# Kernel tuning notes

Measured on AMD Instinct MI355X. Metric: run time of the kernel, lower is better.

The kernel has to match this reference:

```python
import jax, jax.numpy as jnp
import numpy as np


def _binarize(x):
    # sign-binarization with straight-through estimator (matches torch .data trick)
    return x + jax.lax.stop_gradient(jnp.sign(x) - x)


def _conv(x, w):
    # x: NCHW, w: OIHW, stride 1, no padding (padding handled explicitly)
    return jax.lax.conv_general_dilated(
        x, w, window_strides=(1, 1), padding='VALID',
        dimension_numbers=('NCHW', 'OIHW', 'NCHW'))


def _hardtanh(x):
    return jnp.clip(x, -1.0, 1.0)


def _maxpool2(x):
    # 2x2 max pool, stride 2, over spatial dims of NCHW
    return jax.lax.reduce_window(
        x, -jnp.inf, jax.lax.max,
        window_dimensions=(1, 1, 2, 2), window_strides=(1, 1, 2, 2),
        padding='VALID')


def setup_inputs() -> dict:
    key = jax.random.key(0)
    kx, k1, k2, k3, k4 = jax.random.split(key, 5)
    x = jax.random.normal(kx, (32, 3, 512, 512), dtype=jnp.float32)
    w1 = jax.random.normal(k1, (8, 3, 3, 3), dtype=jnp.float32) * 0.1
    w2 = jax.random.normal(k2, (16, 8, 3, 3), dtype=jnp.float32) * 0.1
    w3 = jax.random.normal(k3, (32, 16, 3, 3), dtype=jnp.float32) * 0.1
    w4 = jax.random.normal(k4, (2, 32, 3, 3), dtype=jnp.float32) * 0.1
    return {'x': x, 'w1': w1, 'w2': w2, 'w3': w3, 'w4': w4}


def reference(x, w1, w2, w3, w4):
    # p0: ConstantPad2d(1, value=1)
    h = jnp.pad(x, ((0, 0), (0, 0), (1, 1), (1, 1)), constant_values=1.0)
    # features1: BinarizeConv2d(3,8) -- input has 3 channels so NOT binarized;
    # weights are sign-binarized. Then Hardtanh, MaxPool2d(2,2).
    h = _maxpool2(_hardtanh(_conv(h, _binarize(w1))))          # [B,8,256,256]
    # features2..4: binarize activations (C != 3) and weights, conv, hardtanh
    h = _hardtanh(_conv(_binarize(h), _binarize(w2)))          # [B,16,254,254]
    h = _hardtanh(_conv(_binarize(h), _binarize(w3)))          # [B,32,252,252]
    h = _hardtanh(_conv(_binarize(h), _binarize(w4)))          # [B,2,250,250]
    return h.reshape(h.shape[0], -1)                           # [B, 125000]
```

## Files before the change

kernel.cpp:

```cpp
#include <hip/hip_runtime.h>
#include <hip/hip_bf16.h>
#include <cstdint>


typedef __attribute__((ext_vector_type(2)))  float f32x2;
typedef __attribute__((ext_vector_type(4)))  int int4v;
typedef __attribute__((ext_vector_type(16))) int int16v;

#define WOFF_W2M 0
#define WOFF_W3M 10240
#define WOFF_W4M 20480
#define WOFF_W1D 30720
#define WEIGHTS_BYTES 32768

#define A1_PB (2*256*256*4)
#define A2_PB (4*254*254*4)

__device__ __forceinline__ int fsign(float w) {
    return (w > 0.f) ? 1 : ((w < 0.f) ? -1 : 0);
}

__device__ __forceinline__ void pkfma_lo(f32x2& acc, f32x2 w, f32x2 v) {
    asm("v_pk_fma_f32 %0, %1, %2, %0 op_sel:[0,0,0] op_sel_hi:[1,0,1]"
        : "+v"(acc) : "s"(w), "v"(v));
}
__device__ __forceinline__ void pkfma_hi(f32x2& acc, f32x2 w, f32x2 v) {
    asm("v_pk_fma_f32 %0, %1, %2, %0 op_sel:[0,1,0] op_sel_hi:[1,1,1]"
        : "+v"(acc) : "s"(w), "v"(v));
}

__global__ __launch_bounds__(256) void kprep(const float* __restrict__ w1,
                                             const float* __restrict__ w2,
                                             const float* __restrict__ w3,
                                             const float* __restrict__ w4,
                                             int* __restrict__ w2m,
                                             int* __restrict__ w3m,
                                             int* __restrict__ w4m,
                                             f32x2* __restrict__ w1d) {
    int tid = threadIdx.x;
    int b = blockIdx.x;
    if (b == 0) {
        for (int idx = tid; idx < 576; idx += 256) {
            int t = idx / 64, l = idx % 64;
            int oc = l & 31, icb = (l >> 5) * 16;
            int wd[4] = {0, 0, 0, 0};
            for (int j = 0; j < 16; ++j) {
                int ic = icb + j;
                int s = (oc < 16 && ic < 8) ? fsign(w2[(oc * 8 + ic) * 9 + t]) : 0;
                wd[j >> 2] |= (s & 0xff) << (8 * (j & 3));
            }
            w2m[idx * 4 + 0] = wd[0]; w2m[idx * 4 + 1] = wd[1];
            w2m[idx * 4 + 2] = wd[2]; w2m[idx * 4 + 3] = wd[3];
        }
    } else if (b == 1) {
        for (int idx = tid; idx < 576; idx += 256) {
            int t = idx / 64, l = idx % 64;
            int oc = l & 31, icb = (l >> 5) * 16;
            int wd[4] = {0, 0, 0, 0};
            for (int j = 0; j < 16; ++j) {
                int ic = icb + j;
                int s = (ic < 16) ? fsign(w3[(oc * 16 + ic) * 9 + t]) : 0;
                wd[j >> 2] |= (s & 0xff) << (8 * (j & 3));
            }
            w3m[idx * 4 + 0] = wd[0]; w3m[idx * 4 + 1] = wd[1];
            w3m[idx * 4 + 2] = wd[2]; w3m[idx * 4 + 3] = wd[3];
        }
    } else {
        for (int idx = tid; idx < 576; idx += 256) {
            int t = idx / 64, l = idx % 64;
            int oc = l & 31, icb = (l >> 5) * 16;
            int wd[4] = {0, 0, 0, 0};
            for (int j = 0; j < 16; ++j) {
                int ic = icb + j;
                int s = (oc < 2) ? fsign(w4[(oc * 32 + ic) * 9 + t]) : 0;
                wd[j >> 2] |= (s & 0xff) << (8 * (j & 3));
            }
            w4m[idx * 4 + 0] = wd[0]; w4m[idx * 4 + 1] = wd[1];
            w4m[idx * 4 + 2] = wd[2]; w4m[idx * 4 + 3] = wd[3];
        }
        for (int i = tid; i < 128; i += 256) {
            int op = i / 32, t = i % 32;
            f32x2 pr = {0.f, 0.f};
            if (t < 27) {
                float wa = w1[(2 * op) * 27 + t];
                float wbv = w1[(2 * op + 1) * 27 + t];
                pr[0] = (wa > 0.f) ? 1.f : ((wa < 0.f) ? -1.f : 0.f);
                pr[1] = (wbv > 0.f) ? 1.f : ((wbv < 0.f) ? -1.f : 0.f);
            }
            w1d[i] = pr;
        }
    }
}

__global__ __launch_bounds__(128, 4) void k1(const float* __restrict__ x,
                                             const f32x2* __restrict__ w1d,
                                             uint32_t* __restrict__ a1, int n0) {
    int tx = threadIdx.x;
    int oy = blockIdx.y;
    int ln = blockIdx.z;
    const float* xn = x + (size_t)(n0 + ln) * 3 * 512 * 512;

    int iy0 = 2 * oy - 1;
    int xb  = 4 * tx;

    f32x2 P[3][4][3];

    if (oy > 0 && oy < 255 && tx > 0 && tx < 127) {
#pragma unroll
        for (int ic = 0; ic < 3; ++ic) {
            const float* xc = xn + (size_t)ic * 512 * 512;
#pragma unroll
            for (int r = 0; r < 4; ++r) {
                const float* rp = xc + (size_t)(iy0 + r) * 512 + xb;
                float  lft = rp[-1];
                float4 m   = *(const float4*)rp;
                float  rgt = rp[4];
                P[ic][r][0] = (f32x2){lft, m.x};
                P[ic][r][1] = (f32x2){m.y, m.z};
                P[ic][r][2] = (f32x2){m.w, rgt};
            }
        }
    } else {
        for (int ic = 0; ic < 3; ++ic) {
            const float* xc = xn + (size_t)ic * 512 * 512;
#pragma unroll
            for (int r = 0; r < 4; ++r) {
                int iy = iy0 + r;
                bool yok = ((unsigned)iy < 512u);
                float t[6];
#pragma unroll
                for (int c = 0; c < 6; ++c) {
                    int ix = xb - 1 + c;
                    t[c] = (yok && ((unsigned)ix < 512u))
                               ? xc[(size_t)iy * 512 + ix] : 1.0f;
                }
                P[ic][r][0] = (f32x2){t[0], t[1]};
                P[ic][r][1] = (f32x2){t[2], t[3]};
                P[ic][r][2] = (f32x2){t[4], t[5]};
            }
        }
    }

#define PKTAP(ACC, ROW, COL)                                         \
    do {                                                             \
        if (((COL) & 1) == 0) pkfma_lo(ACC, ww, P[ic][ROW][(COL) >> 1]); \
        else                  pkfma_hi(ACC, ww, P[ic][ROW][(COL) >> 1]); \
    } while (0)

    uint64_t dallA = 0, dallB = 0;
#pragma unroll 1
    for (int op = 0; op < 4; ++op) {
        const f32x2* wb = w1d + op * 32;
        f32x2 wop[27];
#pragma unroll
        for (int t = 0; t < 27; ++t) wop[t] = wb[t];

        f32x2 aA00 = {0.f, 0.f}, aA01 = {0.f, 0.f};
        f32x2 aA10 = {0.f, 0.f}, aA11 = {0.f, 0.f};
        f32x2 aB00 = {0.f, 0.f}, aB01 = {0.f, 0.f};
        f32x2 aB10 = {0.f, 0.f}, aB11 = {0.f, 0.f};
#pragma unroll
        for (int ky = 0; ky < 3; ++ky) {
#pragma unroll
            for (int kx = 0; kx < 3; ++kx) {
#pragma unroll
                for (int ic = 0; ic < 3; ++ic) {
                    f32x2 ww = wop[ic * 9 + ky * 3 + kx];
                    PKTAP(aA00, ky + 0, kx + 0);
                    PKTAP(aA01, ky + 0, kx + 1);
                    PKTAP(aA10, ky + 1, kx + 0);
                    PKTAP(aA11, ky + 1, kx + 1);
                    PKTAP(aB00, ky + 0, kx + 2);
                    PKTAP(aB01, ky + 0, kx + 3);
                    PKTAP(aB10, ky + 1, kx + 2);
                    PKTAP(aB11, ky + 1, kx + 3);
                }
            }
        }
        float mA0 = fmaxf(fmaxf(aA00[0], aA01[0]), fmaxf(aA10[0], aA11[0]));
        float mA1 = fmaxf(fmaxf(aA00[1], aA01[1]), fmaxf(aA10[1], aA11[1]));
        float mB0 = fmaxf(fmaxf(aB00[0], aB01[0]), fmaxf(aB10[0], aB11[0]));
        float mB1 = fmaxf(fmaxf(aB00[1], aB01[1]), fmaxf(aB10[1], aB11[1]));
        int sA0 = (mA0 > 0.f) ? 1 : ((mA0 < 0.f) ? -1 : 0);
        int sA1 = (mA1 > 0.f) ? 1 : ((mA1 < 0.f) ? -1 : 0);
        int sB0 = (mB0 > 0.f) ? 1 : ((mB0 < 0.f) ? -1 : 0);
        int sB1 = (mB1 > 0.f) ? 1 : ((mB1 < 0.f) ? -1 : 0);
        dallA |= (uint64_t)(uint32_t)(sA0 & 0xff) << (8 * (2 * op));
        dallA |= (uint64_t)(uint32_t)(sA1 & 0xff) << (8 * (2 * op + 1));
        dallB |= (uint64_t)(uint32_t)(sB0 & 0xff) << (8 * (2 * op));
        dallB |= (uint64_t)(uint32_t)(sB1 & 0xff) << (8 * (2 * op + 1));
    }
#undef PKTAP

    size_t base = (((size_t)ln * 2) * 256 + oy) * 256 + 2 * tx;
    uint2 v0, v1;
    v0.x = (uint32_t)dallA;         v0.y = (uint32_t)dallB;
    v1.x = (uint32_t)(dallA >> 32); v1.y = (uint32_t)(dallB >> 32);
    *(uint2*)(a1 + base)             = v0;
    *(uint2*)(a1 + base + 256 * 256) = v1;
}

__global__ __launch_bounds__(256) void kconv2(const uint32_t* __restrict__ ain,
                                              const int* __restrict__ wm,
                                              uint32_t* __restrict__ aout) {
    __shared__ uint32_t stb[10][36][2];
    int w    = threadIdx.x >> 6;
    int lane = threadIdx.x & 63;
    int x0 = blockIdx.x * 32;
    int y0 = blockIdx.y * 8;
    int ln = blockIdx.z;

    const int4v* wmv = (const int4v*)wm;
    int4v bfr[9];
#pragma unroll
    for (int t = 0; t < 9; ++t) bfr[t] = wmv[t * 64 + lane];

    const uint32_t* abase = ain + (size_t)ln * 2 * 256 * 256;
    for (int idx = threadIdx.x; idx < 10 * 36 * 2; idx += 256) {
        int icg = idx & 1;
        int r2 = idx >> 1;
        int xx = r2 % 36, row = r2 / 36;
        int gy = y0 + row, gx = x0 + xx;
        uint32_t val = 0;
        if (xx < 34 && gx < 256 && gy < 256)
            val = abase[((size_t)icg * 256 + gy) * 256 + gx];
        stb[row][xx][icg] = val;
    }
    __syncthreads();

    int xl = lane & 31;
    int h  = lane >> 5;

#pragma unroll
    for (int ry = 0; ry < 2; ++ry) {
        int yy = y0 + 2 * w + ry;
        int16v acc = {};
#pragma unroll
        for (int ky = 0; ky < 3; ++ky) {
#pragma unroll
            for (int kx = 0; kx < 3; ++kx) {
                uint32_t d0 = stb[2 * w + ry + ky][xl + kx][0];
                uint32_t d1 = stb[2 * w + ry + ky][xl + kx][1];
                int4v a; a[0] = (int)d0; a[1] = (int)d1; a[2] = 0; a[3] = 0;
                acc = __builtin_amdgcn_mfma_i32_32x32x32_i8(bfr[ky * 3 + kx], a, acc, 0, 0, 0);
            }
        }
        bool ok = (yy < 254) && (x0 + xl < 254);
#pragma unroll
        for (int g = 0; g < 4; ++g) {
            int ocg = 2 * g + h;
            if (ocg < 4 && ok) {
                uint32_t dw = 0;
#pragma unroll
                for (int j = 0; j < 4; ++j) {
                    int v = min(max(acc[4 * g + j], -1), 1);
                    dw |= (uint32_t)(v & 0xff) << (8 * j);
                }
                aout[(((size_t)ln * 4 + ocg) * 254 + yy) * 254 + x0 + xl] = dw;
            }
        }
    }
}

__global__ __launch_bounds__(256) void kconv34(const uint32_t* __restrict__ a2,
                                               const int* __restrict__ w3m,
                                               const int* __restrict__ w4m,
                                               float* __restrict__ out, int n0) {
    __shared__ uint32_t sA2[12][68][4];
    __shared__ uint32_t sA3[10 * 66 * 9];
    int w    = threadIdx.x >> 6;
    int lane = threadIdx.x & 63;
    int xl = lane & 31;
    int h  = lane >> 5;
    int x0 = blockIdx.x * 62;
    int y0 = blockIdx.y * 8;
    int ln = blockIdx.z;

    const int4v* wmv3 = (const int4v*)w3m;
    int4v bfr[9];
#pragma unroll
    for (int t = 0; t < 9; ++t) bfr[t] = wmv3[t * 64 + lane];

    const uint32_t* abase = a2 + (size_t)ln * 4 * 254 * 254;
    for (int idx = threadIdx.x; idx < 12 * 64 * 4; idx += 256) {
        int row = idx >> 8;
        int xx  = (idx >> 2) & 63;
        int icg = idx & 3;
        int gy = y0 + row, gx = x0 + xx;
        uint32_t val = 0;
        if (gy < 254 && gx < 254)
            val = abase[((size_t)icg * 254 + gy) * 254 + gx];
        sA2[row][xx][icg] = val;
    }
    if (threadIdx.x < 96) {
        int row = threadIdx.x >> 3;
        int xx  = 64 + ((threadIdx.x >> 2) & 1);
        int icg = threadIdx.x & 3;
        int gy = y0 + row, gx = x0 + xx;
        uint32_t val = 0;
        if (gy < 254 && gx < 254)
            val = abase[((size_t)icg * 254 + gy) * 254 + gx];
        sA2[row][xx][icg] = val;
    }
    __syncthreads();

#pragma unroll
    for (int t5 = 0; t5 < 5; ++t5) {
        int t = t5 * 4 + w;
        int row = t >> 1, ct = t & 1;
        int16v acc = {};
#pragma unroll
        for (int ky = 0; ky < 3; ++ky) {
#pragma unroll
            for (int kx = 0; kx < 3; ++kx) {
                int4v a = *(const int4v*)&sA2[row + ky][ct * 32 + xl + kx][0];
                acc = __builtin_amdgcn_mfma_i32_32x32x32_i8(bfr[ky * 3 + kx], a, acc, 0, 0, 0);
            }
        }
        int pbase = (row * 66 + ct * 32 + xl) * 9;
#pragma unroll
        for (int g = 0; g < 4; ++g) {
            uint32_t dw = 0;
#pragma unroll
            for (int j = 0; j < 4; ++j) {
                int v = min(max(acc[4 * g + j], -1), 1);
                dw |= (uint32_t)(v & 0xff) << (8 * j);
            }
            sA3[pbase + 2 * g + h] = dw;
        }
    }

    const int4v* wmv4 = (const int4v*)w4m;
    int4v bf4[9];
#pragma unroll
    for (int t = 0; t < 9; ++t) bf4[t] = wmv4[t * 64 + lane];
    __syncthreads();

    size_t gn = (size_t)(n0 + ln);
#pragma unroll
    for (int t4 = 0; t4 < 4; ++t4) {
        int t = t4 * 4 + w;
        int y = t >> 1, ct2 = t & 1;
        int gy = y0 + y;
        int16v acc = {};
#pragma unroll
        for (int ky = 0; ky < 3; ++ky) {
#pragma unroll
            for (int kx = 0; kx < 3; ++kx) {
                const uint32_t* pb = &sA3[((y + ky) * 66 + ct2 * 32 + xl + kx) * 9 + h * 4];
                int4v bv;
                bv[0] = (int)pb[0]; bv[1] = (int)pb[1];
                bv[2] = (int)pb[2]; bv[3] = (int)pb[3];
                acc = __builtin_amdgcn_mfma_i32_32x32x32_i8(bf4[ky * 3 + kx], bv, acc, 0, 0, 0);
            }
        }
        if (h == 0) {
            int lx = ct2 * 32 + xl;
            if (lx < 62 && x0 + lx < 250 && gy < 250) {
                float v0 = fminf(fmaxf((float)acc[0], -1.f), 1.f);
                float v1 = fminf(fmaxf((float)acc[1], -1.f), 1.f);
                out[((gn * 2 + 0) * 250 + gy) * 250 + x0 + lx] = v0;
                out[((gn * 2 + 1) * 250 + gy) * 250 + x0 + lx] = v1;
            }
        }
    }
}

extern "C" void kernel_launch(void* const* d_in, const int* in_sizes, int n_in,
                              void* d_out, int out_size, void* d_ws, size_t ws_size,
                              hipStream_t stream) {
    const float* x  = (const float*)d_in[0];
    const float* w1 = (const float*)d_in[1];
    const float* w2 = (const float*)d_in[2];
    const float* w3 = (const float*)d_in[3];
    const float* w4 = (const float*)d_in[4];
    char* ws = (char*)d_ws;

    int*   w2m = (int*)(ws + WOFF_W2M);
    int*   w3m = (int*)(ws + WOFF_W3M);
    int*   w4m = (int*)(ws + WOFF_W4M);
    f32x2* w1d = (f32x2*)(ws + WOFF_W1D);
    float* out = (float*)d_out;

    size_t per = (size_t)A1_PB + (size_t)A2_PB;
    int NC = 32;
    while (NC > 1 && (size_t)WEIGHTS_BYTES + (size_t)NC * per > ws_size) NC >>= 1;

    uint32_t* A1 = (uint32_t*)(ws + WEIGHTS_BYTES);
    uint32_t* A2 = (uint32_t*)(ws + WEIGHTS_BYTES + (size_t)NC * A1_PB);

    kprep<<<dim3(3), 256, 0, stream>>>(w1, w2, w3, w4, w2m, w3m, w4m, w1d);
    for (int n0 = 0; n0 < 32; n0 += NC) {
        k1<<<dim3(1, 256, NC), 128, 0, stream>>>(x, w1d, A1, n0);
        kconv2<<<dim3(8, 32, NC), 256, 0, stream>>>(A1, w2m, A2);
        kconv34<<<dim3(5, 32, NC), 256, 0, stream>>>(A2, w3m, w4m, out, n0);
    }
}
```

Measured before the change: 140.5 us.

## Store layer-2 activations channel-interleaved and read them directly from global in conv34

Changes the intermediate a2 buffer from planar [icg][y][x] to interleaved [y][x][icg] so each pixel's 16 int8 channels form one contiguous 16-byte vector. The conv34 kernel then drops its shared-memory staging tile and barrier and loads the MFMA A operand straight from global memory (through cache), with a fast path for interior tiles. This removes the LDS fill and sync, at the cost of redundant global and cache loads for overlapping 3x3 windows. The conv2 store loop is also trimmed to the two valid channel groups.

```diff
diff --git a/kernel.cpp b/kernel.cpp
--- a/kernel.cpp
+++ b/kernel.cpp
@@ -14,7 +14,7 @@
 #define WEIGHTS_BYTES 32768
 
 #define A1_PB (2*256*256*4)
-#define A2_PB (4*254*254*4)
+#define A2_PB (254*254*4*4)
 
 __device__ __forceinline__ int fsign(float w) {
     return (w > 0.f) ? 1 : ((w < 0.f) ? -1 : 0);
@@ -230,6 +230,7 @@
 
     int xl = lane & 31;
     int h  = lane >> 5;
+    uint32_t* obase = aout + (size_t)ln * 254 * 254 * 4;
 
 #pragma unroll
     for (int ry = 0; ry < 2; ++ry) {
@@ -247,16 +248,16 @@
         }
         bool ok = (yy < 254) && (x0 + xl < 254);
 #pragma unroll
-        for (int g = 0; g < 4; ++g) {
+        for (int g = 0; g < 2; ++g) {
             int ocg = 2 * g + h;
-            if (ocg < 4 && ok) {
+            if (ok) {
                 uint32_t dw = 0;
 #pragma unroll
                 for (int j = 0; j < 4; ++j) {
                     int v = min(max(acc[4 * g + j], -1), 1);
                     dw |= (uint32_t)(v & 0xff) << (8 * j);
                 }
-                aout[(((size_t)ln * 4 + ocg) * 254 + yy) * 254 + x0 + xl] = dw;
+                obase[((size_t)yy * 254 + x0 + xl) * 4 + ocg] = dw;
             }
         }
     }
@@ -266,7 +267,6 @@
                                                const int* __restrict__ w3m,
                                                const int* __restrict__ w4m,
                                                float* __restrict__ out, int n0) {
-    __shared__ uint32_t sA2[12][68][4];
     __shared__ uint32_t sA3[10 * 66 * 9];
     int w    = threadIdx.x >> 6;
     int lane = threadIdx.x & 63;
@@ -281,28 +281,8 @@
 #pragma unroll
     for (int t = 0; t < 9; ++t) bfr[t] = wmv3[t * 64 + lane];
 
-    const uint32_t* abase = a2 + (size_t)ln * 4 * 254 * 254;
-    for (int idx = threadIdx.x; idx < 12 * 64 * 4; idx += 256) {
-        int row = idx >> 8;
-        int xx  = (idx >> 2) & 63;
-        int icg = idx & 3;
-        int gy = y0 + row, gx = x0 + xx;
-        uint32_t val = 0;
-        if (gy < 254 && gx < 254)
-            val = abase[((size_t)icg * 254 + gy) * 254 + gx];
-        sA2[row][xx][icg] = val;
-    }
-    if (threadIdx.x < 96) {
-        int row = threadIdx.x >> 3;
-        int xx  = 64 + ((threadIdx.x >> 2) & 1);
-        int icg = threadIdx.x & 3;
-        int gy = y0 + row, gx = x0 + xx;
-        uint32_t val = 0;
-        if (gy < 254 && gx < 254)
-            val = abase[((size_t)icg * 254 + gy) * 254 + gx];
-        sA2[row][xx][icg] = val;
-    }
-    __syncthreads();
+    const uint32_t* abase = a2 + (size_t)ln * 254 * 254 * 4;
+    bool interior = (x0 + 65 < 254) && (y0 + 11 < 254);
 
 #pragma unroll
     for (int t5 = 0; t5 < 5; ++t5) {
@@ -313,7 +293,16 @@
         for (int ky = 0; ky < 3; ++ky) {
 #pragma unroll
             for (int kx = 0; kx < 3; ++kx) {
-                int4v a = *(const int4v*)&sA2[row + ky][ct * 32 + xl + kx][0];
+                int gy = y0 + row + ky;
+                int gx = x0 + ct * 32 + xl + kx;
+                int4v a;
+                if (interior) {
+                    a = *(const int4v*)(abase + ((size_t)gy * 254 + gx) * 4);
+                } else if (gy < 254 && gx < 254) {
+                    a = *(const int4v*)(abase + ((size_t)gy * 254 + gx) * 4);
+                } else {
+                    a = (int4v){0, 0, 0, 0};
+                }
                 acc = __builtin_amdgcn_mfma_i32_32x32x32_i8(bfr[ky * 3 + kx], a, acc, 0, 0, 0);
             }
         }
```

Measured after the change: 166.8 us. 1.19x slower.
